# Kernel tuning notes

Measured on AMD Instinct MI355X. Metric: run time of the kernel, lower is better.

Reference implementation:

```python
import jax, jax.numpy as jnp
import numpy as np

N_NODES = 100000
N_EDGES = 1600000
N_GRAPHS = 256
IN_C = 64
HID = 64


def _gcn_conv(x, W, b, src, dst, w, n):
    # GCNConv: x' = D^{-1/2} (A + I) D^{-1/2} (x W) + b, with edge weights w
    x = x @ W
    deg = jnp.zeros((n,), x.dtype).at[dst].add(w) + 1.0  # +1 for self-loop weight
    dinv = jax.lax.rsqrt(deg)
    norm = dinv[src] * w * dinv[dst]                      # [E]
    agg = jnp.zeros_like(x).at[dst].add(x[src] * norm[:, None])
    agg = agg + x * (1.0 / deg)[:, None]                  # self-loop term: d^{-1/2}*1*d^{-1/2}
    return agg + b


def setup_inputs() -> dict:
    key = jax.random.key(0)
    ks = jax.random.split(key, 16)
    inp = {
        "x": jax.random.normal(ks[0], (N_NODES, IN_C), jnp.float32),
        "edge_index": jax.random.randint(ks[1], (2, N_EDGES), 0, N_NODES, jnp.int32),
        "edge_weight": jax.random.uniform(ks[2], (N_EDGES,), jnp.float32),
        "batch": jnp.sort(jax.random.randint(ks[3], (N_NODES,), 0, N_GRAPHS, jnp.int32)),
    }
    s = 0.05
    inp["W0"] = jax.random.normal(ks[4], (IN_C, HID), jnp.float32) * s
    inp["b0"] = jnp.zeros((HID,), jnp.float32)
    inp["W1"] = jax.random.normal(ks[5], (HID, HID), jnp.float32) * s
    inp["b1"] = jnp.zeros((HID,), jnp.float32)
    inp["W2"] = jax.random.normal(ks[6], (HID, HID), jnp.float32) * s
    inp["b2"] = jnp.zeros((HID,), jnp.float32)
    inp["Wr0"] = jax.random.normal(ks[7], (HID, HID // 2), jnp.float32) * s
    inp["br0"] = jnp.zeros((HID // 2,), jnp.float32)
    inp["Wr1"] = jax.random.normal(ks[8], (HID // 2, 1), jnp.float32) * s
    inp["br1"] = jnp.zeros((1,), jnp.float32)
    return inp


def reference(x, edge_index, edge_weight, batch, W0, b0, W1, b1, W2, b2, Wr0, br0, Wr1, br1):
    n = x.shape[0]
    src, dst = edge_index[0], edge_index[1]
    h = jax.nn.relu(_gcn_conv(x, W0, b0, src, dst, edge_weight, n))
    h = jax.nn.relu(_gcn_conv(h, W1, b1, src, dst, edge_weight, n))
    h = _gcn_conv(h, W2, b2, src, dst, edge_weight, n)  # no activation on last GNN layer
    # MLP readout: hidden -> hidden//2 -> 1
    h = jax.nn.relu(h @ Wr0 + br0) @ Wr1 + br1          # [N, 1]
    # scatter-mean pooling by graph id
    sums = jax.ops.segment_sum(h, batch, num_segments=N_GRAPHS)
    cnt = jax.ops.segment_sum(jnp.ones((n, 1), h.dtype), batch, num_segments=N_GRAPHS)
    return sums / jnp.maximum(cnt, 1.0)
```

## Files before the change

### kernel.cpp

```cpp
#include <hip/hip_runtime.h>


#define NBK 391

__device__ __forceinline__ float bcastf(float v, int l) {
    return __int_as_float(__builtin_amdgcn_readlane(__float_as_int(v), l));
}

__global__ void hist_kernel(const int* __restrict__ dst,
                            int* __restrict__ bcnt, int ne) {
    __shared__ int h[512];
    for (int i = threadIdx.x; i < 512; i += blockDim.x) h[i] = 0;
    __syncthreads();
    int stride = gridDim.x * blockDim.x;
    for (int e = blockIdx.x * blockDim.x + threadIdx.x; e < ne; e += stride)
        atomicAdd(&h[dst[e] >> 8], 1);
    __syncthreads();
    for (int i = threadIdx.x; i < 512; i += blockDim.x)
        if (h[i]) atomicAdd(&bcnt[i], h[i]);
}

__global__ void bscan_kernel(const int* __restrict__ bcnt,
                             int* __restrict__ bbase,
                             int* __restrict__ gcur, int nb, int ne) {
    __shared__ int sh[512];
    int t = threadIdx.x;
    int v = (t < nb) ? bcnt[t] : 0;
    sh[t] = v;
    __syncthreads();
    for (int off = 1; off < 512; off <<= 1) {
        int u = (t >= off) ? sh[t - off] : 0;
        __syncthreads();
        sh[t] += u;
        __syncthreads();
    }
    if (t < nb) {
        int e = sh[t] - v;
        bbase[t] = e;
        gcur[t] = e;
    }
    if (t == 0) bbase[nb] = ne;
}

__global__ void scatterB_kernel(const int* __restrict__ src,
                                const int* __restrict__ dst,
                                const float* __restrict__ ew,
                                int* __restrict__ gcur,
                                int2* __restrict__ packed, int ne) {
    __shared__ int h[512];
    __shared__ int cur[512];
    int chunk = (ne + gridDim.x - 1) / gridDim.x;
    int e0 = blockIdx.x * chunk;
    int e1 = e0 + chunk; if (e1 > ne) e1 = ne;
    for (int i = threadIdx.x; i < 512; i += blockDim.x) h[i] = 0;
    __syncthreads();
    for (int e = e0 + threadIdx.x; e < e1; e += blockDim.x)
        atomicAdd(&h[dst[e] >> 8], 1);
    __syncthreads();
    for (int i = threadIdx.x; i < 512; i += blockDim.x)
        cur[i] = h[i] ? atomicAdd(&gcur[i], h[i]) : 0;
    __syncthreads();
    for (int e = e0 + threadIdx.x; e < e1; e += blockDim.x) {
        int d = dst[e];
        int pos = atomicAdd(&cur[d >> 8], 1);
        int2 v;
        v.x = ((d & 255) << 24) | src[e];
        v.y = __float_as_int(ew[e]);
        packed[pos] = v;
    }
}

__global__ void bucket_build_kernel(const int2* __restrict__ packed,
                                    const int* __restrict__ bbase,
                                    int* __restrict__ rptr,
                                    int* __restrict__ cnt,
                                    float* __restrict__ dinv,
                                    int2* __restrict__ csr, int n) {
    __shared__ int cl[256];
    __shared__ int sc[256];
    __shared__ int cur[256];
    int b = blockIdx.x;
    int t = threadIdx.x;
    int node0 = b << 8;
    int nn = n - node0; if (nn > 256) nn = 256;
    int ebase = bbase[b];
    int m = bbase[b + 1] - ebase;
    cl[t] = 0;
    __syncthreads();
    for (int j = t; j < m; j += 256) {
        int local = ((unsigned)packed[ebase + j].x) >> 24;
        atomicAdd(&cl[local], 1);
    }
    __syncthreads();
    int c = cl[t];
    sc[t] = c;
    __syncthreads();
    for (int off = 1; off < 256; off <<= 1) {
        int u = (t >= off) ? sc[t - off] : 0;
        __syncthreads();
        sc[t] += u;
        __syncthreads();
    }
    int base = ebase + sc[t] - c;
    cur[t] = base;
    if (t < nn) {
        rptr[node0 + t] = base;
        cnt[node0 + t] = c;
    }
    __syncthreads();
    for (int j = t; j < m; j += 256) {
        int2 p = packed[ebase + j];
        int local = ((unsigned)p.x) >> 24;
        int pos = atomicAdd(&cur[local], 1);
        int2 v;
        v.x = p.x & 0x00FFFFFF;
        v.y = p.y;
        csr[pos] = v;
    }
    __syncthreads();
    if (t < nn) {
        float s = 0.0f;
        for (int j = base; j < base + c; ++j)
            s += __int_as_float(csr[j].y);
        dinv[node0 + t] = 1.0f / sqrtf(s + 1.0f);
    }
}

template <bool RELU>
__global__ void __launch_bounds__(256, 4)
gemm_rl_kernel(const float* __restrict__ X, const float* W,
               const float* __restrict__ dinv, float* __restrict__ Ts,
               int n) {
    __shared__ float Wl[4096];
    {
        const float4* Wv = (const float4*)W;
        float4* Lv = (float4*)Wl;
        for (int i = threadIdx.x; i < 1024; i += 256) Lv[i] = Wv[i];
    }
    __syncthreads();
    int lane = threadIdx.x & 63;
    int wid  = (blockIdx.x * blockDim.x + threadIdx.x) >> 6;
    int nw   = (gridDim.x * blockDim.x) >> 6;
    int lrow = lane >> 4;
    int lcol = (lane & 15) * 4;
    for (int r0 = wid * 4; r0 + 4 <= n; r0 += nw * 4) {
        float4 xv = *(const float4*)&X[(size_t)(r0 + lrow) * 64 + lcol];
        if (RELU) {
            xv.x = fmaxf(xv.x, 0.f); xv.y = fmaxf(xv.y, 0.f);
            xv.z = fmaxf(xv.z, 0.f); xv.w = fmaxf(xv.w, 0.f);
        }
        float a0 = 0.f, a1 = 0.f, a2 = 0.f, a3 = 0.f;
#pragma unroll
        for (int k4 = 0; k4 < 16; ++k4) {
            float w0 = Wl[(4 * k4 + 0) * 64 + lane];
            float w1 = Wl[(4 * k4 + 1) * 64 + lane];
            float w2 = Wl[(4 * k4 + 2) * 64 + lane];
            float w3 = Wl[(4 * k4 + 3) * 64 + lane];
            a0 = fmaf(bcastf(xv.x, k4), w0, a0);
            a0 = fmaf(bcastf(xv.y, k4), w1, a0);
            a0 = fmaf(bcastf(xv.z, k4), w2, a0);
            a0 = fmaf(bcastf(xv.w, k4), w3, a0);
            a1 = fmaf(bcastf(xv.x, 16 + k4), w0, a1);
            a1 = fmaf(bcastf(xv.y, 16 + k4), w1, a1);
            a1 = fmaf(bcastf(xv.z, 16 + k4), w2, a1);
            a1 = fmaf(bcastf(xv.w, 16 + k4), w3, a1);
            a2 = fmaf(bcastf(xv.x, 32 + k4), w0, a2);
            a2 = fmaf(bcastf(xv.y, 32 + k4), w1, a2);
            a2 = fmaf(bcastf(xv.z, 32 + k4), w2, a2);
            a2 = fmaf(bcastf(xv.w, 32 + k4), w3, a2);
            a3 = fmaf(bcastf(xv.x, 48 + k4), w0, a3);
            a3 = fmaf(bcastf(xv.y, 48 + k4), w1, a3);
            a3 = fmaf(bcastf(xv.z, 48 + k4), w2, a3);
            a3 = fmaf(bcastf(xv.w, 48 + k4), w3, a3);
        }
        Ts[(size_t)(r0 + 0) * 64 + lane] = a0 * dinv[r0 + 0];
        Ts[(size_t)(r0 + 1) * 64 + lane] = a1 * dinv[r0 + 1];
        Ts[(size_t)(r0 + 2) * 64 + lane] = a2 * dinv[r0 + 2];
        Ts[(size_t)(r0 + 3) * 64 + lane] = a3 * dinv[r0 + 3];
    }
    if (wid == 0) {
        for (int r = (n & ~3); r < n; ++r) {
            const float4* xr = (const float4*)(X + (size_t)r * 64);
            float acc = 0.f;
#pragma unroll
            for (int k4 = 0; k4 < 16; ++k4) {
                float4 a = xr[k4];
                if (RELU) {
                    a.x = fmaxf(a.x, 0.f); a.y = fmaxf(a.y, 0.f);
                    a.z = fmaxf(a.z, 0.f); a.w = fmaxf(a.w, 0.f);
                }
                acc = fmaf(a.x, Wl[(4 * k4 + 0) * 64 + lane], acc);
                acc = fmaf(a.y, Wl[(4 * k4 + 1) * 64 + lane], acc);
                acc = fmaf(a.z, Wl[(4 * k4 + 2) * 64 + lane], acc);
                acc = fmaf(a.w, Wl[(4 * k4 + 3) * 64 + lane], acc);
            }
            Ts[(size_t)r * 64 + lane] = acc * dinv[r];
        }
    }
}

__global__ void gather_kernel(const int2* __restrict__ csr,
                              const int* __restrict__ rptr,
                              const int* __restrict__ cnt,
                              const float* __restrict__ dinv,
                              const float* __restrict__ b,
                              const float* __restrict__ Ts,
                              float* __restrict__ A, int n) {
    int lane = threadIdx.x & 63;
    int r = (int)(((size_t)blockIdx.x * blockDim.x + threadIdx.x) >> 6);
    if (r >= n) return;
    int sub = lane >> 4;
    int cl  = lane & 15;
    int start = rptr[r];
    int m = cnt[r];
    float4 a0 = {0.f, 0.f, 0.f, 0.f};
    float4 a1 = {0.f, 0.f, 0.f, 0.f};
    float4 a2 = {0.f, 0.f, 0.f, 0.f};
    float4 a3 = {0.f, 0.f, 0.f, 0.f};
    int j = sub;
    for (; j + 12 < m; j += 16) {
        int2 e0 = csr[start + j];
        int2 e1 = csr[start + j + 4];
        int2 e2 = csr[start + j + 8];
        int2 e3 = csr[start + j + 12];
        float w0 = __int_as_float(e0.y);
        float w1 = __int_as_float(e1.y);
        float w2 = __int_as_float(e2.y);
        float w3 = __int_as_float(e3.y);
        float4 t0 = *(const float4*)&Ts[(size_t)e0.x * 64 + cl * 4];
        float4 t1 = *(const float4*)&Ts[(size_t)e1.x * 64 + cl * 4];
        float4 t2 = *(const float4*)&Ts[(size_t)e2.x * 64 + cl * 4];
        float4 t3 = *(const float4*)&Ts[(size_t)e3.x * 64 + cl * 4];
        a0.x = fmaf(t0.x, w0, a0.x); a0.y = fmaf(t0.y, w0, a0.y);
        a0.z = fmaf(t0.z, w0, a0.z); a0.w = fmaf(t0.w, w0, a0.w);
        a1.x = fmaf(t1.x, w1, a1.x); a1.y = fmaf(t1.y, w1, a1.y);
        a1.z = fmaf(t1.z, w1, a1.z); a1.w = fmaf(t1.w, w1, a1.w);
        a2.x = fmaf(t2.x, w2, a2.x); a2.y = fmaf(t2.y, w2, a2.y);
        a2.z = fmaf(t2.z, w2, a2.z); a2.w = fmaf(t2.w, w2, a2.w);
        a3.x = fmaf(t3.x, w3, a3.x); a3.y = fmaf(t3.y, w3, a3.y);
        a3.z = fmaf(t3.z, w3, a3.z); a3.w = fmaf(t3.w, w3, a3.w);
    }
    for (; j < m; j += 4) {
        int2 e0 = csr[start + j];
        float w0 = __int_as_float(e0.y);
        float4 t0 = *(const float4*)&Ts[(size_t)e0.x * 64 + cl * 4];
        a0.x = fmaf(t0.x, w0, a0.x); a0.y = fmaf(t0.y, w0, a0.y);
        a0.z = fmaf(t0.z, w0, a0.z); a0.w = fmaf(t0.w, w0, a0.w);
    }
    a0.x += a1.x + a2.x + a3.x;
    a0.y += a1.y + a2.y + a3.y;
    a0.z += a1.z + a2.z + a3.z;
    a0.w += a1.w + a2.w + a3.w;
#pragma unroll
    for (int off = 16; off < 64; off <<= 1) {
        a0.x += __shfl_xor(a0.x, off);
        a0.y += __shfl_xor(a0.y, off);
        a0.z += __shfl_xor(a0.z, off);
        a0.w += __shfl_xor(a0.w, off);
    }
    if (sub == 0) {
        float dv = dinv[r];
        float4 ts = *(const float4*)&Ts[(size_t)r * 64 + cl * 4];
        float4 bb = *(const float4*)&b[cl * 4];
        float4 o;
        o.x = fmaf(dv, a0.x + ts.x, bb.x);
        o.y = fmaf(dv, a0.y + ts.y, bb.y);
        o.z = fmaf(dv, a0.z + ts.z, bb.z);
        o.w = fmaf(dv, a0.w + ts.w, bb.w);
        *(float4*)&A[(size_t)r * 64 + cl * 4] = o;
    }
}

__global__ void readout_kernel(const float* __restrict__ H,
                               const float* __restrict__ Wr0,
                               const float* __restrict__ br0,
                               const float* __restrict__ Wr1,
                               const float* __restrict__ br1,
                               const int* __restrict__ batch,
                               float* __restrict__ gsum,
                               float* __restrict__ gcnt, int n) {
    __shared__ float Ws[64 * 32];
    __shared__ float w1s[32];
    for (int i = threadIdx.x; i < 64 * 32; i += blockDim.x) Ws[i] = Wr0[i];
    if (threadIdx.x < 32) w1s[threadIdx.x] = Wr1[threadIdx.x];
    __syncthreads();
    int r = blockIdx.x * blockDim.x + threadIdx.x;
    int lane = threadIdx.x & 63;
    float sv = 0.0f;
    int g = -1;
    if (r < n) {
        float h[64];
        const float4* hr = (const float4*)(H + (size_t)r * 64);
#pragma unroll
        for (int i = 0; i < 16; ++i) {
            float4 v = hr[i];
            h[4 * i + 0] = v.x; h[4 * i + 1] = v.y;
            h[4 * i + 2] = v.z; h[4 * i + 3] = v.w;
        }
        float ssum = 0.0f;
#pragma unroll 1
        for (int jg = 0; jg < 8; ++jg) {
            float a0 = br0[jg * 4 + 0], a1 = br0[jg * 4 + 1];
            float a2 = br0[jg * 4 + 2], a3 = br0[jg * 4 + 3];
#pragma unroll
            for (int k = 0; k < 64; ++k) {
                const float4 wv = *(const float4*)&Ws[k * 32 + jg * 4];
                a0 = fmaf(h[k], wv.x, a0);
                a1 = fmaf(h[k], wv.y, a1);
                a2 = fmaf(h[k], wv.z, a2);
                a3 = fmaf(h[k], wv.w, a3);
            }
            a0 = fmaxf(a0, 0.0f); a1 = fmaxf(a1, 0.0f);
            a2 = fmaxf(a2, 0.0f); a3 = fmaxf(a3, 0.0f);
            ssum += a0 * w1s[jg * 4 + 0] + a1 * w1s[jg * 4 + 1] +
                    a2 * w1s[jg * 4 + 2] + a3 * w1s[jg * 4 + 3];
        }
        sv = ssum + br1[0];
        g = batch[r];
    }
    float c = (r < n) ? 1.0f : 0.0f;
#pragma unroll
    for (int off = 1; off < 64; off <<= 1) {
        int   og = __shfl_down(g, off);
        float ov = __shfl_down(sv, off);
        float oc = __shfl_down(c, off);
        if ((lane + off) < 64 && og == g) { sv += ov; c += oc; }
    }
    int gprev = __shfl_up(g, 1);
    bool head = (lane == 0) || (gprev != g);
    if (head && g >= 0) {
        atomicAdd(&gsum[g], sv);
        atomicAdd(&gcnt[g], c);
    }
}

__global__ void pool_fin_kernel(const float* __restrict__ gsum,
                                const float* __restrict__ gcnt,
                                float* __restrict__ out, int ng) {
    int g = blockIdx.x * blockDim.x + threadIdx.x;
    if (g < ng) out[g] = gsum[g] / fmaxf(gcnt[g], 1.0f);
}

extern "C" void kernel_launch(void* const* d_in, const int* in_sizes, int n_in,
                              void* d_out, int out_size, void* d_ws, size_t ws_size,
                              hipStream_t stream) {
    const float* x    = (const float*)d_in[0];
    const int*   ei   = (const int*)d_in[1];
    const float* ew   = (const float*)d_in[2];
    const int*   batch= (const int*)d_in[3];
    const float* W0   = (const float*)d_in[4];
    const float* b0   = (const float*)d_in[5];
    const float* W1   = (const float*)d_in[6];
    const float* b1   = (const float*)d_in[7];
    const float* W2   = (const float*)d_in[8];
    const float* b2   = (const float*)d_in[9];
    const float* Wr0  = (const float*)d_in[10];
    const float* br0  = (const float*)d_in[11];
    const float* Wr1  = (const float*)d_in[12];
    const float* br1  = (const float*)d_in[13];
    float* out = (float*)d_out;

    int n  = in_sizes[0] / 64;
    int ne = in_sizes[1] / 2;
    int ng = out_size;
    const int* srcv = ei;
    const int* dstv = ei + ne;
    int nbk = (n + 255) >> 8;

    char* ws = (char*)d_ws;
    size_t off = 0;
    auto alloc = [&](size_t bytes) {
        void* p = ws + off;
        off += (bytes + 255) & ~(size_t)255;
        return p;
    };
    float* Ts     = (float*)alloc((size_t)n * 64 * sizeof(float));
    float* A      = (float*)alloc((size_t)n * 64 * sizeof(float));
    float* dinv   = (float*)alloc((size_t)n * sizeof(float));
    int*   cnt    = (int*)alloc((size_t)n * sizeof(int));
    int*   rptr   = (int*)alloc((size_t)n * sizeof(int));
    int*   bcnt   = (int*)alloc(520 * sizeof(int));
    int*   bbase  = (int*)alloc(520 * sizeof(int));
    int*   gcur   = (int*)alloc(520 * sizeof(int));
    int2*  csr    = (int2*)alloc((size_t)ne * sizeof(int2));
    float* gsum   = (float*)alloc((size_t)ng * sizeof(float));
    float* gcnt   = (float*)alloc((size_t)ng * sizeof(float));
    int2*  packed = (int2*)Ts;
    (void)ws_size;

    hipMemsetAsync(bcnt, 0, 520 * sizeof(int), stream);
    hipMemsetAsync(gsum, 0, (size_t)ng * sizeof(float), stream);
    hipMemsetAsync(gcnt, 0, (size_t)ng * sizeof(float), stream);

    hist_kernel<<<256, 256, 0, stream>>>(dstv, bcnt, ne);
    bscan_kernel<<<1, 512, 0, stream>>>(bcnt, bbase, gcur, nbk, ne);
    scatterB_kernel<<<200, 256, 0, stream>>>(srcv, dstv, ew, gcur, packed, ne);
    bucket_build_kernel<<<nbk, 256, 0, stream>>>(packed, bbase, rptr, cnt,
                                                 dinv, csr, n);

    const int gemm_blocks = 2048;
    unsigned gat_blocks = (unsigned)(((size_t)n * 64 + 255) / 256);

    gemm_rl_kernel<false><<<gemm_blocks, 256, 0, stream>>>(x, W0, dinv, Ts, n);
    gather_kernel<<<gat_blocks, 256, 0, stream>>>(csr, rptr, cnt, dinv, b0, Ts, A, n);

    gemm_rl_kernel<true><<<gemm_blocks, 256, 0, stream>>>(A, W1, dinv, Ts, n);
    gather_kernel<<<gat_blocks, 256, 0, stream>>>(csr, rptr, cnt, dinv, b1, Ts, A, n);

    gemm_rl_kernel<true><<<gemm_blocks, 256, 0, stream>>>(A, W2, dinv, Ts, n);
    gather_kernel<<<gat_blocks, 256, 0, stream>>>(csr, rptr, cnt, dinv, b2, Ts, A, n);

    readout_kernel<<<(n + 255) / 256, 256, 0, stream>>>(A, Wr0, br0, Wr1, br1,
                                                        batch, gsum, gcnt, n);
    pool_fin_kernel<<<(ng + 255) / 256, 256, 0, stream>>>(gsum, gcnt, out, ng);
}
```

Measured before the change: 385.8 us.

## Fuse next-layer GEMM into gather epilogue for hidden GCN layers

```diff
diff --git a/kernel.cpp b/kernel.cpp
--- a/kernel.cpp
+++ b/kernel.cpp
@@ -197,6 +197,92 @@
             Ts[(size_t)r * 64 + lane] = acc * dinv[r];
         }
     }
+}
+
+__global__ void __launch_bounds__(256, 4)
+fgather_kernel(const int2* __restrict__ csr,
+               const int* __restrict__ rptr,
+               const int* __restrict__ cnt,
+               const float* __restrict__ dinv,
+               const float* __restrict__ b,
+               const float* __restrict__ Ts_in,
+               const float* Wn,
+               float* __restrict__ Ts_out, int n) {
+    __shared__ float Wl[4096];
+    {
+        const float4* Wv = (const float4*)Wn;
+        float4* Lv = (float4*)Wl;
+        for (int i = threadIdx.x; i < 1024; i += 256) Lv[i] = Wv[i];
+    }
+    __syncthreads();
+    int lane = threadIdx.x & 63;
+    int r = (int)(((size_t)blockIdx.x * blockDim.x + threadIdx.x) >> 6);
+    if (r >= n) return;
+    int sub = lane >> 4;
+    int cl  = lane & 15;
+    int start = rptr[r];
+    int m = cnt[r];
+    float4 a0 = {0.f, 0.f, 0.f, 0.f};
+    float4 a1 = {0.f, 0.f, 0.f, 0.f};
+    float4 a2 = {0.f, 0.f, 0.f, 0.f};
+    float4 a3 = {0.f, 0.f, 0.f, 0.f};
+    int j = sub;
+    for (; j + 12 < m; j += 16) {
+        int2 e0 = csr[start + j];
+        int2 e1 = csr[start + j + 4];
+        int2 e2 = csr[start + j + 8];
+        int2 e3 = csr[start + j + 12];
+        float w0 = __int_as_float(e0.y);
+        float w1 = __int_as_float(e1.y);
+        float w2 = __int_as_float(e2.y);
+        float w3 = __int_as_float(e3.y);
+        float4 t0 = *(const float4*)&Ts_in[(size_t)e0.x * 64 + cl * 4];
+        float4 t1 = *(const float4*)&Ts_in[(size_t)e1.x * 64 + cl * 4];
+        float4 t2 = *(const float4*)&Ts_in[(size_t)e2.x * 64 + cl * 4];
+        float4 t3 = *(const float4*)&Ts_in[(size_t)e3.x * 64 + cl * 4];
+        a0.x = fmaf(t0.x, w0, a0.x); a0.y = fmaf(t0.y, w0, a0.y);
+        a0.z = fmaf(t0.z, w0, a0.z); a0.w = fmaf(t0.w, w0, a0.w);
+        a1.x = fmaf(t1.x, w1, a1.x); a1.y = fmaf(t1.y, w1, a1.y);
+        a1.z = fmaf(t1.z, w1, a1.z); a1.w = fmaf(t1.w, w1, a1.w);
+        a2.x = fmaf(t2.x, w2, a2.x); a2.y = fmaf(t2.y, w2, a2.y);
+        a2.z = fmaf(t2.z, w2, a2.z); a2.w = fmaf(t2.w, w2, a2.w);
+        a3.x = fmaf(t3.x, w3, a3.x); a3.y = fmaf(t3.y, w3, a3.y);
+        a3.z = fmaf(t3.z, w3, a3.z); a3.w = fmaf(t3.w, w3, a3.w);
+    }
+    for (; j < m; j += 4) {
+        int2 e0 = csr[start + j];
+        float w0 = __int_as_float(e0.y);
+        float4 t0 = *(const float4*)&Ts_in[(size_t)e0.x * 64 + cl * 4];
+        a0.x = fmaf(t0.x, w0, a0.x); a0.y = fmaf(t0.y, w0, a0.y);
+        a0.z = fmaf(t0.z, w0, a0.z); a0.w = fmaf(t0.w, w0, a0.w);
+    }
+    a0.x += a1.x + a2.x + a3.x;
+    a0.y += a1.y + a2.y + a3.y;
+    a0.z += a1.z + a2.z + a3.z;
+    a0.w += a1.w + a2.w + a3.w;
+#pragma unroll
+    for (int off = 16; off < 64; off <<= 1) {
+        a0.x += __shfl_xor(a0.x, off);
+        a0.y += __shfl_xor(a0.y, off);
+        a0.z += __shfl_xor(a0.z, off);
+        a0.w += __shfl_xor(a0.w, off);
+    }
+    float dv = dinv[r];
+    float4 ts = *(const float4*)&Ts_in[(size_t)r * 64 + cl * 4];
+    float4 bb = *(const float4*)&b[cl * 4];
+    float tx = fmaxf(fmaf(dv, a0.x + ts.x, bb.x), 0.f);
+    float ty = fmaxf(fmaf(dv, a0.y + ts.y, bb.y), 0.f);
+    float tz = fmaxf(fmaf(dv, a0.z + ts.z, bb.z), 0.f);
+    float tw = fmaxf(fmaf(dv, a0.w + ts.w, bb.w), 0.f);
+    float acc = 0.f;
+#pragma unroll
+    for (int q = 0; q < 16; ++q) {
+        acc = fmaf(bcastf(tx, q), Wl[(4 * q + 0) * 64 + lane], acc);
+        acc = fmaf(bcastf(ty, q), Wl[(4 * q + 1) * 64 + lane], acc);
+        acc = fmaf(bcastf(tz, q), Wl[(4 * q + 2) * 64 + lane], acc);
+        acc = fmaf(bcastf(tw, q), Wl[(4 * q + 3) * 64 + lane], acc);
+    }
+    Ts_out[(size_t)r * 64 + lane] = acc * dv;
 }
 
 __global__ void gather_kernel(const int2* __restrict__ csr,
@@ -402,13 +488,12 @@
     unsigned gat_blocks = (unsigned)(((size_t)n * 64 + 255) / 256);
 
     gemm_rl_kernel<false><<<gemm_blocks, 256, 0, stream>>>(x, W0, dinv, Ts, n);
-    gather_kernel<<<gat_blocks, 256, 0, stream>>>(csr, rptr, cnt, dinv, b0, Ts, A, n);
-
-    gemm_rl_kernel<true><<<gemm_blocks, 256, 0, stream>>>(A, W1, dinv, Ts, n);
-    gather_kernel<<<gat_blocks, 256, 0, stream>>>(csr, rptr, cnt, dinv, b1, Ts, A, n);
-
-    gemm_rl_kernel<true><<<gemm_blocks, 256, 0, stream>>>(A, W2, dinv, Ts, n);
-    gather_kernel<<<gat_blocks, 256, 0, stream>>>(csr, rptr, cnt, dinv, b2, Ts, A, n);
+    fgather_kernel<<<gat_blocks, 256, 0, stream>>>(csr, rptr, cnt, dinv, b0,
+                                                   Ts, W1, A, n);
+    fgather_kernel<<<gat_blocks, 256, 0, stream>>>(csr, rptr, cnt, dinv, b1,
+                                                   A, W2, Ts, n);
+    gather_kernel<<<gat_blocks, 256, 0, stream>>>(csr, rptr, cnt, dinv, b2,
+                                                  Ts, A, n);
 
     readout_kernel<<<(n + 255) / 256, 256, 0, stream>>>(A, Wr0, br0, Wr1, br1,
                                                         batch, gsum, gcnt, n);
```

Result: faster. 359.7 us (-6.8%).
